# Kernel optimization log

Measured on AMD Instinct MI355X. Metric: run time of the kernel, lower is better.

Reference implementation:

```python
import jax, jax.numpy as jnp
import numpy as np

N = 50000
E = 800000
IN_DIM = 128
HIDDEN = 256
HEADS = 8
HEAD_DIM = HIDDEN // HEADS  # 32
NUM_CLASSES = 40
NEG_SLOPE = 0.2


def setup_inputs() -> dict:
    key = jax.random.key(0)
    ks = jax.random.split(key, 16)
    x = jax.random.normal(ks[0], (N, IN_DIM), dtype=jnp.float32)
    edge_index = jax.random.randint(ks[1], (2, E), 0, N, dtype=jnp.int64)

    def glorot(k, shape, fan_in):
        return jax.random.normal(k, shape, dtype=jnp.float32) / np.sqrt(fan_in)

    # layer 1: in -> heads*head_dim (concat)
    W1 = glorot(ks[2], (IN_DIM, HEADS * HEAD_DIM), IN_DIM)
    as1 = glorot(ks[3], (HEADS, HEAD_DIM), HEAD_DIM)
    ad1 = glorot(ks[4], (HEADS, HEAD_DIM), HEAD_DIM)
    b1 = jnp.zeros((HEADS * HEAD_DIM,), dtype=jnp.float32)
    # layer 2: hidden -> heads*head_dim (concat)
    W2 = glorot(ks[5], (HIDDEN, HEADS * HEAD_DIM), HIDDEN)
    as2 = glorot(ks[6], (HEADS, HEAD_DIM), HEAD_DIM)
    ad2 = glorot(ks[7], (HEADS, HEAD_DIM), HEAD_DIM)
    b2 = jnp.zeros((HEADS * HEAD_DIM,), dtype=jnp.float32)
    # layer 3: hidden -> num_classes, 1 head, no concat (mean == identity for 1 head)
    W3 = glorot(ks[8], (HIDDEN, 1 * NUM_CLASSES), HIDDEN)
    as3 = glorot(ks[9], (1, NUM_CLASSES), NUM_CLASSES)
    ad3 = glorot(ks[10], (1, NUM_CLASSES), NUM_CLASSES)
    b3 = jnp.zeros((NUM_CLASSES,), dtype=jnp.float32)
    return {"x": x, "edge_index": edge_index,
            "W1": W1, "as1": as1, "ad1": ad1, "b1": b1,
            "W2": W2, "as2": as2, "ad2": ad2, "b2": b2,
            "W3": W3, "as3": as3, "ad3": ad3, "b3": b3}


def _segment_softmax(logits, seg, n):
    # logits: [E, H]; softmax per destination node
    m = jax.ops.segment_max(logits, seg, num_segments=n)
    m = jnp.where(jnp.isfinite(m), m, 0.0)  # empty segments -> 0
    e = jnp.exp(logits - m[seg])
    s = jax.ops.segment_sum(e, seg, num_segments=n)
    return e / (s[seg] + 1e-16)


def _gat_layer(x, src, dst, W, a_src, a_dst, b, heads, concat):
    n = x.shape[0]
    h = (x @ W).reshape(n, heads, -1)                    # [N, H, D]
    al_s = jnp.einsum('nhd,hd->nh', h, a_src)            # [N, H]
    al_d = jnp.einsum('nhd,hd->nh', h, a_dst)            # [N, H]
    e = jax.nn.leaky_relu(al_s[src] + al_d[dst], NEG_SLOPE)  # [E, H]
    alpha = _segment_softmax(e, dst, n)                  # [E, H]
    msg = h[src] * alpha[..., None]                      # [E, H, D]
    out = jax.ops.segment_sum(msg, dst, num_segments=n)  # [N, H, D]
    out = out.reshape(n, -1) if concat else out.mean(axis=1)
    return out + b


def reference(x, edge_index, W1, as1, ad1, b1, W2, as2, ad2, b2, W3, as3, ad3, b3):
    # add self loops (PyG GATConv default)
    loops = jnp.arange(N, dtype=edge_index.dtype)
    src = jnp.concatenate([edge_index[0], loops])
    dst = jnp.concatenate([edge_index[1], loops])
    # eval mode: dropout is a no-op
    h = _gat_layer(x, src, dst, W1, as1, ad1, b1, HEADS, True)
    h = jax.nn.elu(h)
    h = _gat_layer(h, src, dst, W2, as2, ad2, b2, HEADS, True)
    h = jax.nn.elu(h)
    out = _gat_layer(h, src, dst, W3, as3, ad3, b3, 1, False)
    return out
```

## Files before the change

kernel.cpp:

```cpp
#include <hip/hip_runtime.h>
#include <hip/hip_bf16.h>

#define NEG_SLOPE 0.2f

typedef __attribute__((ext_vector_type(8))) short bf16x8;
typedef __attribute__((ext_vector_type(4))) float f32x4;

__device__ __forceinline__ unsigned short f2bf(float v) {
    union { float f; unsigned int u; } x; x.f = v;
    unsigned int r = x.u + 0x7fffu + ((x.u >> 16) & 1u);
    return (unsigned short)(r >> 16);
}
__device__ __forceinline__ float bf2f(unsigned short b) {
    union { unsigned int u; float f; } x; x.u = ((unsigned int)b) << 16;
    return x.f;
}


__global__ void count_edges_k(const int* __restrict__ ei, int E, int n, int* __restrict__ cnt) {
    int e = blockIdx.x * 256 + threadIdx.x;
    int ET = E + n;
    if (e >= ET) return;
    int d = (e < E) ? ei[E + e] : (e - E);
    atomicAdd(&cnt[d], 1);
}

__global__ void scan1_k(const int* __restrict__ cnt, int* __restrict__ row_ptr,
                        int* __restrict__ bsums, int n) {
    __shared__ int sd[256];
    int b = blockIdx.x, t = threadIdx.x;
    int base = b * 1024 + t * 4;
    int v[4];
    int loc = 0;
#pragma unroll
    for (int j = 0; j < 4; ++j) {
        v[j] = (base + j < n) ? cnt[base + j] : 0;
        loc += v[j];
    }
    sd[t] = loc;
    __syncthreads();
    for (int off = 1; off < 256; off <<= 1) {
        int x = (t >= off) ? sd[t - off] : 0;
        __syncthreads();
        sd[t] += x;
        __syncthreads();
    }
    int run = sd[t] - loc;
    if (t == 255) bsums[b] = sd[t];
#pragma unroll
    for (int j = 0; j < 4; ++j) {
        if (base + j < n) row_ptr[base + j] = run;
        run += v[j];
    }
}

__global__ void scan2_k(int* __restrict__ bsums, int nb) {
    __shared__ int sd[256];
    int t = threadIdx.x;
    int val = (t < nb) ? bsums[t] : 0;
    sd[t] = val;
    __syncthreads();
    for (int off = 1; off < 256; off <<= 1) {
        int x = (t >= off) ? sd[t - off] : 0;
        __syncthreads();
        sd[t] += x;
        __syncthreads();
    }
    if (t < nb) bsums[t] = sd[t] - val;
}

__global__ void scan3_k(int* __restrict__ row_ptr, int* __restrict__ pos,
                        const int* __restrict__ bsums, int n, int total) {
    int idx = blockIdx.x * 256 + threadIdx.x;
    if (idx < n) {
        int vv = row_ptr[idx] + bsums[idx >> 10];
        row_ptr[idx] = vv;
        pos[idx] = vv;
    } else if (idx == n) {
        row_ptr[n] = total;
    }
}

__global__ void scatter_edges_k(const int* __restrict__ ei, int E, int n,
                                int* __restrict__ pos, int* __restrict__ srcs) {
    int e = blockIdx.x * 256 + threadIdx.x;
    int ET = E + n;
    if (e >= ET) return;
    int s, d;
    if (e < E) { s = ei[e]; d = ei[E + e]; }
    else       { s = e - E; d = e - E; }
    int idx = atomicAdd(&pos[d], 1);
    srcs[idx] = s;
}


#define R1 (128 * 256)
#define R2 (256 * 256)
#define R3 (256 * 128)

__global__ void convert_w_all_k(const float* __restrict__ W1, const float* __restrict__ W2,
                                const float* __restrict__ W3,
                                unsigned short* __restrict__ b1h, unsigned short* __restrict__ b1l,
                                unsigned short* __restrict__ b2h, unsigned short* __restrict__ b2l,
                                unsigned short* __restrict__ b3h, unsigned short* __restrict__ b3l) {
    int idx = blockIdx.x * 256 + threadIdx.x;
    float v;
    unsigned short* dh;
    unsigned short* dl;
    int o;
    if (idx < R1) {
        int k = idx >> 8, c = idx & 255;
        v = W1[idx]; dh = b1h; dl = b1l; o = c * 128 + k;
    } else if (idx < R1 + R2) {
        int j = idx - R1;
        int k = j >> 8, c = j & 255;
        v = W2[j]; dh = b2h; dl = b2l; o = c * 256 + k;
    } else if (idx < R1 + R2 + R3) {
        int j = idx - (R1 + R2);
        int k = j >> 7, c = j & 127;
        v = (c < 40) ? W3[k * 40 + c] : 0.f;
        dh = b3h; dl = b3l; o = c * 256 + k;
    } else {
        return;
    }
    unsigned short h = f2bf(v);
    dh[o] = h;
    dl[o] = f2bf(v - bf2f(h));
}


#define GPAD 40

__global__ __launch_bounds__(256) void mfma_gemm_k(const float* __restrict__ A,
                                                   const unsigned short* __restrict__ Bh,
                                                   const unsigned short* __restrict__ Bl,
                                                   unsigned short* __restrict__ Cb,
                                                   int M, int K, int Nc) {
    __shared__ unsigned short Ash[128][GPAD];
    __shared__ unsigned short Asl[128][GPAD];
    __shared__ unsigned short Bsh[128][GPAD];
    __shared__ unsigned short Bsl[128][GPAD];

    int bm = blockIdx.y * 128;
    int bn = blockIdx.x * 128;
    int t = threadIdx.x;
    int w = t >> 6, l = t & 63;
    int wm = w >> 1, wn = w & 1;
    int lr = l & 15, lk = (l >> 4) * 8;

    int srow = t >> 1;
    int skh  = (t & 1) * 16;

    f32x4 acc[4][4];
#pragma unroll
    for (int i = 0; i < 4; ++i)
#pragma unroll
        for (int j = 0; j < 4; ++j)
            acc[i][j] = (f32x4){0.f, 0.f, 0.f, 0.f};

    const int arow = bm + srow;
    const bool arow_ok = (arow < M);
    const size_t acol_base = (size_t)arow * K + skh;
    const size_t bcol_base = (size_t)(bn + srow) * K + skh;

    for (int k0 = 0; k0 < K; k0 += 32) {
        float vv[16];
        if (arow_ok) {
            const float4* ap = reinterpret_cast<const float4*>(A + acol_base + k0);
#pragma unroll
            for (int q = 0; q < 4; ++q) {
                float4 v4 = ap[q];
                vv[4 * q + 0] = v4.x; vv[4 * q + 1] = v4.y;
                vv[4 * q + 2] = v4.z; vv[4 * q + 3] = v4.w;
            }
        } else {
#pragma unroll
            for (int q = 0; q < 16; ++q) vv[q] = 0.f;
        }
        unsigned int hw[8], lw[8];
#pragma unroll
        for (int q = 0; q < 8; ++q) {
            unsigned short h0 = f2bf(vv[2 * q]);
            unsigned short h1 = f2bf(vv[2 * q + 1]);
            unsigned short l0 = f2bf(vv[2 * q] - bf2f(h0));
            unsigned short l1 = f2bf(vv[2 * q + 1] - bf2f(h1));
            hw[q] = (unsigned int)h0 | ((unsigned int)h1 << 16);
            lw[q] = (unsigned int)l0 | ((unsigned int)l1 << 16);
        }
        __syncthreads();
        {
            uint4* dh = reinterpret_cast<uint4*>(&Ash[srow][skh]);
            uint4* dl = reinterpret_cast<uint4*>(&Asl[srow][skh]);
            dh[0] = make_uint4(hw[0], hw[1], hw[2], hw[3]);
            dh[1] = make_uint4(hw[4], hw[5], hw[6], hw[7]);
            dl[0] = make_uint4(lw[0], lw[1], lw[2], lw[3]);
            dl[1] = make_uint4(lw[4], lw[5], lw[6], lw[7]);
        }
        {
            const uint4* sh = reinterpret_cast<const uint4*>(Bh + bcol_base + k0);
            const uint4* sl = reinterpret_cast<const uint4*>(Bl + bcol_base + k0);
            uint4* dh = reinterpret_cast<uint4*>(&Bsh[srow][skh]);
            uint4* dl = reinterpret_cast<uint4*>(&Bsl[srow][skh]);
            dh[0] = sh[0]; dh[1] = sh[1];
            dl[0] = sl[0]; dl[1] = sl[1];
        }
        __syncthreads();

        bf16x8 ah[4], al[4], bh[4], bl[4];
#pragma unroll
        for (int i = 0; i < 4; ++i) {
            int r = wm * 64 + i * 16 + lr;
            ah[i] = *reinterpret_cast<const bf16x8*>(&Ash[r][lk]);
            al[i] = *reinterpret_cast<const bf16x8*>(&Asl[r][lk]);
        }
#pragma unroll
        for (int j = 0; j < 4; ++j) {
            int c = wn * 64 + j * 16 + lr;
            bh[j] = *reinterpret_cast<const bf16x8*>(&Bsh[c][lk]);
            bl[j] = *reinterpret_cast<const bf16x8*>(&Bsl[c][lk]);
        }
#pragma unroll
        for (int i = 0; i < 4; ++i)
#pragma unroll
            for (int j = 0; j < 4; ++j) {
                acc[i][j] = __builtin_amdgcn_mfma_f32_16x16x32_bf16(ah[i], bh[j], acc[i][j], 0, 0, 0);
                acc[i][j] = __builtin_amdgcn_mfma_f32_16x16x32_bf16(ah[i], bl[j], acc[i][j], 0, 0, 0);
                acc[i][j] = __builtin_amdgcn_mfma_f32_16x16x32_bf16(al[i], bh[j], acc[i][j], 0, 0, 0);
            }
    }

#pragma unroll
    for (int i = 0; i < 4; ++i) {
#pragma unroll
        for (int r = 0; r < 4; ++r) {
            int row_g = bm + wm * 64 + i * 16 + (l >> 4) * 4 + r;
            if (row_g >= M) continue;
#pragma unroll
            for (int j = 0; j < 4; ++j) {
                int col_g = bn + wn * 64 + j * 16 + lr;
                Cb[(size_t)row_g * Nc + col_g] = f2bf(acc[i][j][r]);
            }
        }
    }
}


__global__ __launch_bounds__(256) void gemm_bf16a_k(const unsigned short* __restrict__ A,
                                                    const unsigned short* __restrict__ Bh,
                                                    const unsigned short* __restrict__ Bl,
                                                    unsigned short* __restrict__ Cb,
                                                    int M, int K, int Nc) {
    __shared__ unsigned short As[128][GPAD];
    __shared__ unsigned short Bsh[128][GPAD];
    __shared__ unsigned short Bsl[128][GPAD];

    int bm = blockIdx.y * 128;
    int bn = blockIdx.x * 128;
    int t = threadIdx.x;
    int w = t >> 6, l = t & 63;
    int wm = w >> 1, wn = w & 1;
    int lr = l & 15, lk = (l >> 4) * 8;

    int srow = t >> 1;
    int skh  = (t & 1) * 16;

    f32x4 acc[4][4];
#pragma unroll
    for (int i = 0; i < 4; ++i)
#pragma unroll
        for (int j = 0; j < 4; ++j)
            acc[i][j] = (f32x4){0.f, 0.f, 0.f, 0.f};

    const int arow = bm + srow;
    const bool arow_ok = (arow < M);
    const size_t acol_base = (size_t)arow * K + skh;
    const size_t bcol_base = (size_t)(bn + srow) * K + skh;

    for (int k0 = 0; k0 < K; k0 += 32) {
        __syncthreads();
        {
            uint4* da = reinterpret_cast<uint4*>(&As[srow][skh]);
            if (arow_ok) {
                const uint4* sa = reinterpret_cast<const uint4*>(A + acol_base + k0);
                da[0] = sa[0]; da[1] = sa[1];
            } else {
                da[0] = make_uint4(0u, 0u, 0u, 0u);
                da[1] = make_uint4(0u, 0u, 0u, 0u);
            }
            const uint4* sh = reinterpret_cast<const uint4*>(Bh + bcol_base + k0);
            const uint4* sl = reinterpret_cast<const uint4*>(Bl + bcol_base + k0);
            uint4* dh = reinterpret_cast<uint4*>(&Bsh[srow][skh]);
            uint4* dl = reinterpret_cast<uint4*>(&Bsl[srow][skh]);
            dh[0] = sh[0]; dh[1] = sh[1];
            dl[0] = sl[0]; dl[1] = sl[1];
        }
        __syncthreads();

        bf16x8 ah[4], bh[4], bl[4];
#pragma unroll
        for (int i = 0; i < 4; ++i) {
            int r = wm * 64 + i * 16 + lr;
            ah[i] = *reinterpret_cast<const bf16x8*>(&As[r][lk]);
        }
#pragma unroll
        for (int j = 0; j < 4; ++j) {
            int c = wn * 64 + j * 16 + lr;
            bh[j] = *reinterpret_cast<const bf16x8*>(&Bsh[c][lk]);
            bl[j] = *reinterpret_cast<const bf16x8*>(&Bsl[c][lk]);
        }
#pragma unroll
        for (int i = 0; i < 4; ++i)
#pragma unroll
            for (int j = 0; j < 4; ++j) {
                acc[i][j] = __builtin_amdgcn_mfma_f32_16x16x32_bf16(ah[i], bh[j], acc[i][j], 0, 0, 0);
                acc[i][j] = __builtin_amdgcn_mfma_f32_16x16x32_bf16(ah[i], bl[j], acc[i][j], 0, 0, 0);
            }
    }

#pragma unroll
    for (int i = 0; i < 4; ++i) {
#pragma unroll
        for (int r = 0; r < 4; ++r) {
            int row_g = bm + wm * 64 + i * 16 + (l >> 4) * 4 + r;
            if (row_g >= M) continue;
#pragma unroll
            for (int j = 0; j < 4; ++j) {
                int col_g = bn + wn * 64 + j * 16 + lr;
                Cb[(size_t)row_g * Nc + col_g] = f2bf(acc[i][j][r]);
            }
        }
    }
}


__global__ __launch_bounds__(256) void compute_al_k(const unsigned short* __restrict__ h,
                                                    const float* __restrict__ a_src,
                                                    const float* __restrict__ a_dst,
                                                    float* __restrict__ al_s,
                                                    float* __restrict__ al_d, int n) {
    int gw = blockIdx.x * 4 + (threadIdx.x >> 6);
    int nw = gridDim.x * 4;
    int lane = threadIdx.x & 63;
    float4 asv = reinterpret_cast<const float4*>(a_src)[lane];
    float4 adv = reinterpret_cast<const float4*>(a_dst)[lane];
    for (int node = gw; node < n; node += nw) {
        ushort4 v = reinterpret_cast<const ushort4*>(h + (size_t)node * 256)[lane];
        float ps = bf2f(v.x) * asv.x + bf2f(v.y) * asv.y + bf2f(v.z) * asv.z + bf2f(v.w) * asv.w;
        float pd = bf2f(v.x) * adv.x + bf2f(v.y) * adv.y + bf2f(v.z) * adv.z + bf2f(v.w) * adv.w;
#pragma unroll
        for (int off = 1; off < 8; off <<= 1) {
            ps += __shfl_xor(ps, off, 64);
            pd += __shfl_xor(pd, off, 64);
        }
        if ((lane & 7) == 0) {
            al_s[node * 8 + (lane >> 3)] = ps;
            al_d[node * 8 + (lane >> 3)] = pd;
        }
    }
}

__global__ __launch_bounds__(256) void compute_al3_k(const unsigned short* __restrict__ h,
                                                     const float* __restrict__ a_src,
                                                     const float* __restrict__ a_dst,
                                                     float* __restrict__ al_s,
                                                     float* __restrict__ al_d, int n) {
    int gw = blockIdx.x * 4 + (threadIdx.x >> 6);
    int nw = gridDim.x * 4;
    int lane = threadIdx.x & 63;
    float as = (lane < 40) ? a_src[lane] : 0.f;
    float ad = (lane < 40) ? a_dst[lane] : 0.f;
    for (int node = gw; node < n; node += nw) {
        float hv = (lane < 40) ? bf2f(h[(size_t)node * 128 + lane]) : 0.f;
        float ps = hv * as;
        float pd = hv * ad;
#pragma unroll
        for (int off = 32; off; off >>= 1) {
            ps += __shfl_xor(ps, off, 64);
            pd += __shfl_xor(pd, off, 64);
        }
        if (lane == 0) { al_s[node] = ps; al_d[node] = pd; }
    }
}


__global__ __launch_bounds__(256) void edge_softmax_k(const float* __restrict__ al_s,
                                                      const float* __restrict__ al_d,
                                                      const int* __restrict__ row_ptr,
                                                      const int* __restrict__ srcs,
                                                      float* __restrict__ w,
                                                      float* __restrict__ inv, int n8) {
    int tid = blockIdx.x * 256 + threadIdx.x;
    if (tid >= n8) return;
    int dst = tid >> 3, hd = tid & 7;
    int beg = row_ptr[dst], end = row_ptr[dst + 1];
    float ald = al_d[tid];

    float m = -1e30f;
    int i = beg;
    for (; i + 2 <= end; i += 2) {
        int s0 = srcs[i], s1 = srcs[i + 1];
        float l0 = al_s[s0 * 8 + hd] + ald;
        float l1 = al_s[s1 * 8 + hd] + ald;
        l0 = (l0 > 0.f) ? l0 : NEG_SLOPE * l0;
        l1 = (l1 > 0.f) ? l1 : NEG_SLOPE * l1;
        m = fmaxf(m, fmaxf(l0, l1));
    }
    if (i < end) {
        int s0 = srcs[i];
        float l0 = al_s[s0 * 8 + hd] + ald;
        l0 = (l0 > 0.f) ? l0 : NEG_SLOPE * l0;
        m = fmaxf(m, l0);
    }

    float sw = 0.f;
    i = beg;
    for (; i + 2 <= end; i += 2) {
        int s0 = srcs[i], s1 = srcs[i + 1];
        float l0 = al_s[s0 * 8 + hd] + ald;
        float l1 = al_s[s1 * 8 + hd] + ald;
        l0 = (l0 > 0.f) ? l0 : NEG_SLOPE * l0;
        l1 = (l1 > 0.f) ? l1 : NEG_SLOPE * l1;
        float e0 = __expf(l0 - m);
        float e1 = __expf(l1 - m);
        w[(size_t)i * 8 + hd] = e0;
        w[(size_t)(i + 1) * 8 + hd] = e1;
        sw += e0 + e1;
    }
    if (i < end) {
        int s = srcs[i];
        float l = al_s[s * 8 + hd] + ald;
        l = (l > 0.f) ? l : NEG_SLOPE * l;
        float e = __expf(l - m);
        w[(size_t)i * 8 + hd] = e;
        sw += e;
    }
    inv[tid] = 1.f / (sw + 1e-16f);
}

__global__ __launch_bounds__(256) void edge_softmax3_k(const float* __restrict__ al_s,
                                                       const float* __restrict__ al_d,
                                                       const int* __restrict__ row_ptr,
                                                       const int* __restrict__ srcs,
                                                       float* __restrict__ w,
                                                       float* __restrict__ inv, int n) {
    int dst = blockIdx.x * 256 + threadIdx.x;
    if (dst >= n) return;
    int beg = row_ptr[dst], end = row_ptr[dst + 1];
    float ald = al_d[dst];

    float m = -1e30f;
    int i = beg;
    for (; i + 2 <= end; i += 2) {
        int s0 = srcs[i], s1 = srcs[i + 1];
        float l0 = al_s[s0] + ald;
        float l1 = al_s[s1] + ald;
        l0 = (l0 > 0.f) ? l0 : NEG_SLOPE * l0;
        l1 = (l1 > 0.f) ? l1 : NEG_SLOPE * l1;
        m = fmaxf(m, fmaxf(l0, l1));
    }
    if (i < end) {
        int s0 = srcs[i];
        float l0 = al_s[s0] + ald;
        l0 = (l0 > 0.f) ? l0 : NEG_SLOPE * l0;
        m = fmaxf(m, l0);
    }

    float sw = 0.f;
    for (i = beg; i < end; ++i) {
        int s = srcs[i];
        float l = al_s[s] + ald;
        l = (l > 0.f) ? l : NEG_SLOPE * l;
        float e = __expf(l - m);
        w[i] = e;
        sw += e;
    }
    inv[dst] = 1.f / (sw + 1e-16f);
}


template <bool ELU>
__global__ __launch_bounds__(256) void gat_gather_k(const unsigned short* __restrict__ h,
                                                    const float* __restrict__ w,
                                                    const float* __restrict__ inv,
                                                    const int* __restrict__ row_ptr,
                                                    const int* __restrict__ srcs,
                                                    const float* __restrict__ bias,
                                                    unsigned short* __restrict__ out, int n) {
    int gw = blockIdx.x * 4 + (threadIdx.x >> 6);
    int nw = gridDim.x * 4;
    int lane = threadIdx.x & 63;
    int hd = lane >> 3;
    const ushort4* hp = reinterpret_cast<const ushort4*>(h);
    float4 b4 = reinterpret_cast<const float4*>(bias)[lane];

    for (int dst = gw; dst < n; dst += nw) {
        int beg = row_ptr[dst], end = row_ptr[dst + 1];
        float4 acc = make_float4(0.f, 0.f, 0.f, 0.f);
        int i = beg;
        for (; i + 4 <= end; i += 4) {
            int s0 = srcs[i + 0], s1 = srcs[i + 1], s2 = srcs[i + 2], s3 = srcs[i + 3];
            float w0 = w[(size_t)(i + 0) * 8 + hd];
            float w1 = w[(size_t)(i + 1) * 8 + hd];
            float w2 = w[(size_t)(i + 2) * 8 + hd];
            float w3 = w[(size_t)(i + 3) * 8 + hd];
            ushort4 v0 = hp[(size_t)s0 * 64 + lane];
            ushort4 v1 = hp[(size_t)s1 * 64 + lane];
            ushort4 v2 = hp[(size_t)s2 * 64 + lane];
            ushort4 v3 = hp[(size_t)s3 * 64 + lane];
            acc.x = fmaf(w0, bf2f(v0.x), acc.x);
            acc.y = fmaf(w0, bf2f(v0.y), acc.y);
            acc.z = fmaf(w0, bf2f(v0.z), acc.z);
            acc.w = fmaf(w0, bf2f(v0.w), acc.w);
            acc.x = fmaf(w1, bf2f(v1.x), acc.x);
            acc.y = fmaf(w1, bf2f(v1.y), acc.y);
            acc.z = fmaf(w1, bf2f(v1.z), acc.z);
            acc.w = fmaf(w1, bf2f(v1.w), acc.w);
            acc.x = fmaf(w2, bf2f(v2.x), acc.x);
            acc.y = fmaf(w2, bf2f(v2.y), acc.y);
            acc.z = fmaf(w2, bf2f(v2.z), acc.z);
            acc.w = fmaf(w2, bf2f(v2.w), acc.w);
            acc.x = fmaf(w3, bf2f(v3.x), acc.x);
            acc.y = fmaf(w3, bf2f(v3.y), acc.y);
            acc.z = fmaf(w3, bf2f(v3.z), acc.z);
            acc.w = fmaf(w3, bf2f(v3.w), acc.w);
        }
        for (; i < end; ++i) {
            int s = srcs[i];
            float wgt = w[(size_t)i * 8 + hd];
            ushort4 v = hp[(size_t)s * 64 + lane];
            acc.x = fmaf(wgt, bf2f(v.x), acc.x);
            acc.y = fmaf(wgt, bf2f(v.y), acc.y);
            acc.z = fmaf(wgt, bf2f(v.z), acc.z);
            acc.w = fmaf(wgt, bf2f(v.w), acc.w);
        }

        float iv = inv[dst * 8 + hd];
        float4 o;
        o.x = acc.x * iv + b4.x;
        o.y = acc.y * iv + b4.y;
        o.z = acc.z * iv + b4.z;
        o.w = acc.w * iv + b4.w;
        if (ELU) {
            o.x = (o.x > 0.f) ? o.x : expm1f(o.x);
            o.y = (o.y > 0.f) ? o.y : expm1f(o.y);
            o.z = (o.z > 0.f) ? o.z : expm1f(o.z);
            o.w = (o.w > 0.f) ? o.w : expm1f(o.w);
        }
        ushort4 ob;
        ob.x = f2bf(o.x); ob.y = f2bf(o.y); ob.z = f2bf(o.z); ob.w = f2bf(o.w);
        reinterpret_cast<ushort4*>(out + (size_t)dst * 256)[lane] = ob;
    }
}

__global__ __launch_bounds__(256) void gat_gather3_k(const unsigned short* __restrict__ h,
                                                     const float* __restrict__ w,
                                                     const float* __restrict__ inv,
                                                     const int* __restrict__ row_ptr,
                                                     const int* __restrict__ srcs,
                                                     const float* __restrict__ bias,
                                                     float* __restrict__ out, int n) {
    int gw = blockIdx.x * 4 + (threadIdx.x >> 6);
    int nw = gridDim.x * 4;
    int lane = threadIdx.x & 63;
    int es = lane >> 4, cl = lane & 15;

    for (int dst = gw; dst < n; dst += nw) {
        int beg = row_ptr[dst], end = row_ptr[dst + 1];
        float4 acc = make_float4(0.f, 0.f, 0.f, 0.f);
        for (int i = beg; i < end; i += 4) {
            int idx = i + es;
            bool ok = (idx < end);
            int s = ok ? srcs[idx] : srcs[beg];
            float wgt = ok ? w[idx] : 0.f;
            ushort4 v = reinterpret_cast<const ushort4*>(h + (size_t)s * 128)[cl];
            acc.x = fmaf(wgt, bf2f(v.x), acc.x);
            acc.y = fmaf(wgt, bf2f(v.y), acc.y);
            acc.z = fmaf(wgt, bf2f(v.z), acc.z);
            acc.w = fmaf(wgt, bf2f(v.w), acc.w);
        }
#pragma unroll
        for (int off = 16; off <= 32; off <<= 1) {
            acc.x += __shfl_xor(acc.x, off, 64);
            acc.y += __shfl_xor(acc.y, off, 64);
            acc.z += __shfl_xor(acc.z, off, 64);
            acc.w += __shfl_xor(acc.w, off, 64);
        }
        if (es == 0 && cl < 10) {
            float iv = inv[dst];
            int c = cl * 4;
            float4 b4 = *reinterpret_cast<const float4*>(bias + c);
            float4 o;
            o.x = acc.x * iv + b4.x;
            o.y = acc.y * iv + b4.y;
            o.z = acc.z * iv + b4.z;
            o.w = acc.w * iv + b4.w;
            *reinterpret_cast<float4*>(out + (size_t)dst * 40 + c) = o;
        }
    }
}


extern "C" void kernel_launch(void* const* d_in, const int* in_sizes, int n_in,
                              void* d_out, int out_size, void* d_ws, size_t ws_size,
                              hipStream_t stream) {
    const float* x   = (const float*)d_in[0];
    const int*   ei  = (const int*)d_in[1];
    const float* W1  = (const float*)d_in[2];
    const float* as1 = (const float*)d_in[3];
    const float* ad1 = (const float*)d_in[4];
    const float* b1  = (const float*)d_in[5];
    const float* W2  = (const float*)d_in[6];
    const float* as2 = (const float*)d_in[7];
    const float* ad2 = (const float*)d_in[8];
    const float* b2  = (const float*)d_in[9];
    const float* W3  = (const float*)d_in[10];
    const float* as3 = (const float*)d_in[11];
    const float* ad3 = (const float*)d_in[12];
    const float* b3  = (const float*)d_in[13];

    const int N = in_sizes[0] / 128;
    const int E = in_sizes[1] / 2;
    const int ET = E + N;

    char* ws = (char*)d_ws;
    size_t off = 0;
    auto alloc = [&](size_t bytes) -> void* {
        void* p = ws + off;
        off += (bytes + 255) & ~(size_t)255;
        return p;
    };
    int*   row_ptr = (int*)alloc(sizeof(int) * (N + 1));
    int*   pos     = (int*)alloc(sizeof(int) * N);
    int*   srcs    = (int*)alloc(sizeof(int) * ET);
    int*   bsums   = (int*)alloc(sizeof(int) * 256);
    float* als     = (float*)alloc(sizeof(float) * N * 8);
    float* ald     = (float*)alloc(sizeof(float) * N * 8);
    float* wbuf    = (float*)alloc(sizeof(float) * (size_t)ET * 8);
    float* invb    = (float*)alloc(sizeof(float) * N * 8);
    unsigned short* hb16 = (unsigned short*)alloc(sizeof(unsigned short) * (size_t)N * 256);
    unsigned short* ab16 = (unsigned short*)alloc(sizeof(unsigned short) * (size_t)N * 256);
    unsigned short* wb1h = (unsigned short*)alloc(sizeof(unsigned short) * 128 * 256);
    unsigned short* wb1l = (unsigned short*)alloc(sizeof(unsigned short) * 128 * 256);
    unsigned short* wb2h = (unsigned short*)alloc(sizeof(unsigned short) * 256 * 256);
    unsigned short* wb2l = (unsigned short*)alloc(sizeof(unsigned short) * 256 * 256);
    unsigned short* wb3h = (unsigned short*)alloc(sizeof(unsigned short) * 128 * 256);
    unsigned short* wb3l = (unsigned short*)alloc(sizeof(unsigned short) * 128 * 256);
    (void)ws_size;

    const int nb = (N + 1023) / 1024;
    const int PG = 2048;

    convert_w_all_k<<<(R1 + R2 + R3 + 255) / 256, 256, 0, stream>>>(
        W1, W2, W3, wb1h, wb1l, wb2h, wb2l, wb3h, wb3l);

    hipMemsetAsync(pos, 0, sizeof(int) * N, stream);
    count_edges_k<<<(ET + 255) / 256, 256, 0, stream>>>(ei, E, N, pos);
    scan1_k<<<nb, 256, 0, stream>>>(pos, row_ptr, bsums, N);
    scan2_k<<<1, 256, 0, stream>>>(bsums, nb);
    scan3_k<<<(N + 1 + 255) / 256, 256, 0, stream>>>(row_ptr, pos, bsums, N, ET);
    scatter_edges_k<<<(ET + 255) / 256, 256, 0, stream>>>(ei, E, N, pos, srcs);

    const int gy = (N + 127) / 128;
    const int gsm = (N * 8 + 255) / 256;

    mfma_gemm_k<<<dim3(2, gy), 256, 0, stream>>>(x, wb1h, wb1l, hb16, N, 128, 256);
    compute_al_k<<<PG, 256, 0, stream>>>(hb16, as1, ad1, als, ald, N);
    edge_softmax_k<<<gsm, 256, 0, stream>>>(als, ald, row_ptr, srcs, wbuf, invb, N * 8);
    gat_gather_k<true><<<PG, 256, 0, stream>>>(hb16, wbuf, invb, row_ptr, srcs, b1, ab16, N);

    gemm_bf16a_k<<<dim3(2, gy), 256, 0, stream>>>(ab16, wb2h, wb2l, hb16, N, 256, 256);
    compute_al_k<<<PG, 256, 0, stream>>>(hb16, as2, ad2, als, ald, N);
    edge_softmax_k<<<gsm, 256, 0, stream>>>(als, ald, row_ptr, srcs, wbuf, invb, N * 8);
    gat_gather_k<true><<<PG, 256, 0, stream>>>(hb16, wbuf, invb, row_ptr, srcs, b2, ab16, N);

    gemm_bf16a_k<<<dim3(1, gy), 256, 0, stream>>>(ab16, wb3h, wb3l, hb16, N, 256, 128);
    compute_al3_k<<<PG, 256, 0, stream>>>(hb16, as3, ad3, als, ald, N);
    edge_softmax3_k<<<(N + 255) / 256, 256, 0, stream>>>(als, ald, row_ptr, srcs, wbuf, invb, N);
    gat_gather3_k<<<PG, 256, 0, stream>>>(hb16, wbuf, invb, row_ptr, srcs, b3, (float*)d_out, N);
}
```

Before: 425.4 us.

## Fuse edge softmax into neighbor gather kernels for all GAT layers

Removes the separate edge_softmax kernels and computes attention logits, the segment max, exponentials and normalization inside the gather kernels. Within each wavefront, 8 lanes per head compute edge weights in parallel and broadcast source indices and weights by shuffle, and the 8 neighbor row loads are batched per step. This drops the E×8 weight buffer write and read plus the inverse-sum buffer and three launches, at the cost of reading al_s twice per edge and extra shuffles.

```diff
diff --git a/kernel.cpp b/kernel.cpp
--- a/kernel.cpp
+++ b/kernel.cpp
@@ -383,158 +383,91 @@
 }
 
 
-__global__ __launch_bounds__(256) void edge_softmax_k(const float* __restrict__ al_s,
-                                                      const float* __restrict__ al_d,
-                                                      const int* __restrict__ row_ptr,
-                                                      const int* __restrict__ srcs,
-                                                      float* __restrict__ w,
-                                                      float* __restrict__ inv, int n8) {
-    int tid = blockIdx.x * 256 + threadIdx.x;
-    if (tid >= n8) return;
-    int dst = tid >> 3, hd = tid & 7;
-    int beg = row_ptr[dst], end = row_ptr[dst + 1];
-    float ald = al_d[tid];
-
-    float m = -1e30f;
-    int i = beg;
-    for (; i + 2 <= end; i += 2) {
-        int s0 = srcs[i], s1 = srcs[i + 1];
-        float l0 = al_s[s0 * 8 + hd] + ald;
-        float l1 = al_s[s1 * 8 + hd] + ald;
-        l0 = (l0 > 0.f) ? l0 : NEG_SLOPE * l0;
-        l1 = (l1 > 0.f) ? l1 : NEG_SLOPE * l1;
-        m = fmaxf(m, fmaxf(l0, l1));
-    }
-    if (i < end) {
-        int s0 = srcs[i];
-        float l0 = al_s[s0 * 8 + hd] + ald;
-        l0 = (l0 > 0.f) ? l0 : NEG_SLOPE * l0;
-        m = fmaxf(m, l0);
-    }
-
-    float sw = 0.f;
-    i = beg;
-    for (; i + 2 <= end; i += 2) {
-        int s0 = srcs[i], s1 = srcs[i + 1];
-        float l0 = al_s[s0 * 8 + hd] + ald;
-        float l1 = al_s[s1 * 8 + hd] + ald;
-        l0 = (l0 > 0.f) ? l0 : NEG_SLOPE * l0;
-        l1 = (l1 > 0.f) ? l1 : NEG_SLOPE * l1;
-        float e0 = __expf(l0 - m);
-        float e1 = __expf(l1 - m);
-        w[(size_t)i * 8 + hd] = e0;
-        w[(size_t)(i + 1) * 8 + hd] = e1;
-        sw += e0 + e1;
-    }
-    if (i < end) {
-        int s = srcs[i];
-        float l = al_s[s * 8 + hd] + ald;
-        l = (l > 0.f) ? l : NEG_SLOPE * l;
-        float e = __expf(l - m);
-        w[(size_t)i * 8 + hd] = e;
-        sw += e;
-    }
-    inv[tid] = 1.f / (sw + 1e-16f);
-}
-
-__global__ __launch_bounds__(256) void edge_softmax3_k(const float* __restrict__ al_s,
-                                                       const float* __restrict__ al_d,
-                                                       const int* __restrict__ row_ptr,
-                                                       const int* __restrict__ srcs,
-                                                       float* __restrict__ w,
-                                                       float* __restrict__ inv, int n) {
-    int dst = blockIdx.x * 256 + threadIdx.x;
-    if (dst >= n) return;
-    int beg = row_ptr[dst], end = row_ptr[dst + 1];
-    float ald = al_d[dst];
-
-    float m = -1e30f;
-    int i = beg;
-    for (; i + 2 <= end; i += 2) {
-        int s0 = srcs[i], s1 = srcs[i + 1];
-        float l0 = al_s[s0] + ald;
-        float l1 = al_s[s1] + ald;
-        l0 = (l0 > 0.f) ? l0 : NEG_SLOPE * l0;
-        l1 = (l1 > 0.f) ? l1 : NEG_SLOPE * l1;
-        m = fmaxf(m, fmaxf(l0, l1));
-    }
-    if (i < end) {
-        int s0 = srcs[i];
-        float l0 = al_s[s0] + ald;
-        l0 = (l0 > 0.f) ? l0 : NEG_SLOPE * l0;
-        m = fmaxf(m, l0);
-    }
-
-    float sw = 0.f;
-    for (i = beg; i < end; ++i) {
-        int s = srcs[i];
-        float l = al_s[s] + ald;
-        l = (l > 0.f) ? l : NEG_SLOPE * l;
-        float e = __expf(l - m);
-        w[i] = e;
-        sw += e;
-    }
-    inv[dst] = 1.f / (sw + 1e-16f);
-}
-
-
 template <bool ELU>
-__global__ __launch_bounds__(256) void gat_gather_k(const unsigned short* __restrict__ h,
-                                                    const float* __restrict__ w,
-                                                    const float* __restrict__ inv,
-                                                    const int* __restrict__ row_ptr,
-                                                    const int* __restrict__ srcs,
-                                                    const float* __restrict__ bias,
-                                                    unsigned short* __restrict__ out, int n) {
+__global__ __launch_bounds__(256) void gat_gather_fused_k(const unsigned short* __restrict__ h,
+                                                          const float* __restrict__ al_s,
+                                                          const float* __restrict__ al_d,
+                                                          const int* __restrict__ row_ptr,
+                                                          const int* __restrict__ srcs,
+                                                          const float* __restrict__ bias,
+                                                          unsigned short* __restrict__ out, int n) {
     int gw = blockIdx.x * 4 + (threadIdx.x >> 6);
     int nw = gridDim.x * 4;
     int lane = threadIdx.x & 63;
-    int hd = lane >> 3;
+    int hd = lane >> 3, sl = lane & 7;
+    int gbase = lane & 56;
     const ushort4* hp = reinterpret_cast<const ushort4*>(h);
     float4 b4 = reinterpret_cast<const float4*>(bias)[lane];
 
     for (int dst = gw; dst < n; dst += nw) {
         int beg = row_ptr[dst], end = row_ptr[dst + 1];
+        float ald = al_d[dst * 8 + hd];
+
+        float m = -1e30f;
+        for (int i = beg + sl; i < end; i += 8) {
+            int s = srcs[i];
+            float l = al_s[s * 8 + hd] + ald;
+            l = (l > 0.f) ? l : NEG_SLOPE * l;
+            m = fmaxf(m, l);
+        }
+        m = fmaxf(m, __shfl_xor(m, 1, 64));
+        m = fmaxf(m, __shfl_xor(m, 2, 64));
+        m = fmaxf(m, __shfl_xor(m, 4, 64));
+
         float4 acc = make_float4(0.f, 0.f, 0.f, 0.f);
-        int i = beg;
-        for (; i + 4 <= end; i += 4) {
-            int s0 = srcs[i + 0], s1 = srcs[i + 1], s2 = srcs[i + 2], s3 = srcs[i + 3];
-            float w0 = w[(size_t)(i + 0) * 8 + hd];
-            float w1 = w[(size_t)(i + 1) * 8 + hd];
-            float w2 = w[(size_t)(i + 2) * 8 + hd];
-            float w3 = w[(size_t)(i + 3) * 8 + hd];
-            ushort4 v0 = hp[(size_t)s0 * 64 + lane];
-            ushort4 v1 = hp[(size_t)s1 * 64 + lane];
-            ushort4 v2 = hp[(size_t)s2 * 64 + lane];
-            ushort4 v3 = hp[(size_t)s3 * 64 + lane];
-            acc.x = fmaf(w0, bf2f(v0.x), acc.x);
-            acc.y = fmaf(w0, bf2f(v0.y), acc.y);
-            acc.z = fmaf(w0, bf2f(v0.z), acc.z);
-            acc.w = fmaf(w0, bf2f(v0.w), acc.w);
-            acc.x = fmaf(w1, bf2f(v1.x), acc.x);
-            acc.y = fmaf(w1, bf2f(v1.y), acc.y);
-            acc.z = fmaf(w1, bf2f(v1.z), acc.z);
-            acc.w = fmaf(w1, bf2f(v1.w), acc.w);
-            acc.x = fmaf(w2, bf2f(v2.x), acc.x);
-            acc.y = fmaf(w2, bf2f(v2.y), acc.y);
-            acc.z = fmaf(w2, bf2f(v2.z), acc.z);
-            acc.w = fmaf(w2, bf2f(v2.w), acc.w);
-            acc.x = fmaf(w3, bf2f(v3.x), acc.x);
-            acc.y = fmaf(w3, bf2f(v3.y), acc.y);
-            acc.z = fmaf(w3, bf2f(v3.z), acc.z);
-            acc.w = fmaf(w3, bf2f(v3.w), acc.w);
-        }
-        for (; i < end; ++i) {
-            int s = srcs[i];
-            float wgt = w[(size_t)i * 8 + hd];
-            ushort4 v = hp[(size_t)s * 64 + lane];
-            acc.x = fmaf(wgt, bf2f(v.x), acc.x);
-            acc.y = fmaf(wgt, bf2f(v.y), acc.y);
-            acc.z = fmaf(wgt, bf2f(v.z), acc.z);
-            acc.w = fmaf(wgt, bf2f(v.w), acc.w);
-        }
-
-        float iv = inv[dst * 8 + hd];
+        float sw = 0.f;
+        int nfull = (end - beg) >> 3;
+        int i0 = beg;
+        for (int b = 0; b < nfull; ++b, i0 += 8) {
+            int sE = srcs[i0 + sl];
+            float l = al_s[sE * 8 + hd] + ald;
+            l = (l > 0.f) ? l : NEG_SLOPE * l;
+            float we = __expf(l - m);
+            sw += we;
+            int sj[8];
+            float wj[8];
+#pragma unroll
+            for (int j = 0; j < 8; ++j) {
+                sj[j] = __shfl(sE, gbase + j, 64);
+                wj[j] = __shfl(we, gbase + j, 64);
+            }
+            ushort4 v[8];
+#pragma unroll
+            for (int j = 0; j < 8; ++j) v[j] = hp[(size_t)sj[j] * 64 + lane];
+#pragma unroll
+            for (int j = 0; j < 8; ++j) {
+                acc.x = fmaf(wj[j], bf2f(v[j].x), acc.x);
+                acc.y = fmaf(wj[j], bf2f(v[j].y), acc.y);
+                acc.z = fmaf(wj[j], bf2f(v[j].z), acc.z);
+                acc.w = fmaf(wj[j], bf2f(v[j].w), acc.w);
+            }
+        }
+        int rem = end - i0;
+        if (rem > 0) {
+            int idx = i0 + sl;
+            int sE = srcs[(idx < end) ? idx : (end - 1)];
+            float we = 0.f;
+            if (idx < end) {
+                float l = al_s[sE * 8 + hd] + ald;
+                l = (l > 0.f) ? l : NEG_SLOPE * l;
+                we = __expf(l - m);
+                sw += we;
+            }
+            for (int j = 0; j < rem; ++j) {
+                int sj = __shfl(sE, gbase + j, 64);
+                float wjv = __shfl(we, gbase + j, 64);
+                ushort4 v = hp[(size_t)sj * 64 + lane];
+                acc.x = fmaf(wjv, bf2f(v.x), acc.x);
+                acc.y = fmaf(wjv, bf2f(v.y), acc.y);
+                acc.z = fmaf(wjv, bf2f(v.z), acc.z);
+                acc.w = fmaf(wjv, bf2f(v.w), acc.w);
+            }
+        }
+
+        sw += __shfl_xor(sw, 1, 64);
+        sw += __shfl_xor(sw, 2, 64);
+        sw += __shfl_xor(sw, 4, 64);
+        float iv = 1.f / (sw + 1e-16f);
         float4 o;
         o.x = acc.x * iv + b4.x;
         o.y = acc.y * iv + b4.y;
@@ -552,13 +485,13 @@
     }
 }
 
-__global__ __launch_bounds__(256) void gat_gather3_k(const unsigned short* __restrict__ h,
-                                                     const float* __restrict__ w,
-                                                     const float* __restrict__ inv,
-                                                     const int* __restrict__ row_ptr,
-                                                     const int* __restrict__ srcs,
-                                                     const float* __restrict__ bias,
-                                                     float* __restrict__ out, int n) {
+__global__ __launch_bounds__(256) void gat_gather3_fused_k(const unsigned short* __restrict__ h,
+                                                           const float* __restrict__ al_s,
+                                                           const float* __restrict__ al_d,
+                                                           const int* __restrict__ row_ptr,
+                                                           const int* __restrict__ srcs,
+                                                           const float* __restrict__ bias,
+                                                           float* __restrict__ out, int n) {
     int gw = blockIdx.x * 4 + (threadIdx.x >> 6);
     int nw = gridDim.x * 4;
     int lane = threadIdx.x & 63;
@@ -566,17 +499,36 @@
 
     for (int dst = gw; dst < n; dst += nw) {
         int beg = row_ptr[dst], end = row_ptr[dst + 1];
+        float ald = al_d[dst];
+
+        float m = -1e30f;
+        for (int i = beg + lane; i < end; i += 64) {
+            int s = srcs[i];
+            float l = al_s[s] + ald;
+            l = (l > 0.f) ? l : NEG_SLOPE * l;
+            m = fmaxf(m, l);
+        }
+#pragma unroll
+        for (int off = 32; off; off >>= 1) m = fmaxf(m, __shfl_xor(m, off, 64));
+
         float4 acc = make_float4(0.f, 0.f, 0.f, 0.f);
+        float sw = 0.f;
         for (int i = beg; i < end; i += 4) {
             int idx = i + es;
             bool ok = (idx < end);
             int s = ok ? srcs[idx] : srcs[beg];
-            float wgt = ok ? w[idx] : 0.f;
+            float we = 0.f;
+            if (ok) {
+                float l = al_s[s] + ald;
+                l = (l > 0.f) ? l : NEG_SLOPE * l;
+                we = __expf(l - m);
+                if (cl == 0) sw += we;
+            }
             ushort4 v = reinterpret_cast<const ushort4*>(h + (size_t)s * 128)[cl];
-            acc.x = fmaf(wgt, bf2f(v.x), acc.x);
-            acc.y = fmaf(wgt, bf2f(v.y), acc.y);
-            acc.z = fmaf(wgt, bf2f(v.z), acc.z);
-            acc.w = fmaf(wgt, bf2f(v.w), acc.w);
+            acc.x = fmaf(we, bf2f(v.x), acc.x);
+            acc.y = fmaf(we, bf2f(v.y), acc.y);
+            acc.z = fmaf(we, bf2f(v.z), acc.z);
+            acc.w = fmaf(we, bf2f(v.w), acc.w);
         }
 #pragma unroll
         for (int off = 16; off <= 32; off <<= 1) {
@@ -585,8 +537,11 @@
             acc.z += __shfl_xor(acc.z, off, 64);
             acc.w += __shfl_xor(acc.w, off, 64);
         }
+#pragma unroll
+        for (int off = 1; off <= 32; off <<= 1) sw += __shfl_xor(sw, off, 64);
+
         if (es == 0 && cl < 10) {
-            float iv = inv[dst];
+            float iv = 1.f / (sw + 1e-16f);
             int c = cl * 4;
             float4 b4 = *reinterpret_cast<const float4*>(bias + c);
             float4 o;
@@ -635,8 +590,6 @@
     int*   bsums   = (int*)alloc(sizeof(int) * 256);
     float* als     = (float*)alloc(sizeof(float) * N * 8);
     float* ald     = (float*)alloc(sizeof(float) * N * 8);
-    float* wbuf    = (float*)alloc(sizeof(float) * (size_t)ET * 8);
-    float* invb    = (float*)alloc(sizeof(float) * N * 8);
     unsigned short* hb16 = (unsigned short*)alloc(sizeof(unsigned short) * (size_t)N * 256);
     unsigned short* ab16 = (unsigned short*)alloc(sizeof(unsigned short) * (size_t)N * 256);
     unsigned short* wb1h = (unsigned short*)alloc(sizeof(unsigned short) * 128 * 256);
@@ -661,20 +614,16 @@
     scatter_edges_k<<<(ET + 255) / 256, 256, 0, stream>>>(ei, E, N, pos, srcs);
 
     const int gy = (N + 127) / 128;
-    const int gsm = (N * 8 + 255) / 256;
 
     mfma_gemm_k<<<dim3(2, gy), 256, 0, stream>>>(x, wb1h, wb1l, hb16, N, 128, 256);
     compute_al_k<<<PG, 256, 0, stream>>>(hb16, as1, ad1, als, ald, N);
-    edge_softmax_k<<<gsm, 256, 0, stream>>>(als, ald, row_ptr, srcs, wbuf, invb, N * 8);
-    gat_gather_k<true><<<PG, 256, 0, stream>>>(hb16, wbuf, invb, row_ptr, srcs, b1, ab16, N);
+    gat_gather_fused_k<true><<<PG, 256, 0, stream>>>(hb16, als, ald, row_ptr, srcs, b1, ab16, N);
 
     gemm_bf16a_k<<<dim3(2, gy), 256, 0, stream>>>(ab16, wb2h, wb2l, hb16, N, 256, 256);
     compute_al_k<<<PG, 256, 0, stream>>>(hb16, as2, ad2, als, ald, N);
-    edge_softmax_k<<<gsm, 256, 0, stream>>>(als, ald, row_ptr, srcs, wbuf, invb, N * 8);
-    gat_gather_k<true><<<PG, 256, 0, stream>>>(hb16, wbuf, invb, row_ptr, srcs, b2, ab16, N);
+    gat_gather_fused_k<true><<<PG, 256, 0, stream>>>(hb16, als, ald, row_ptr, srcs, b2, ab16, N);
 
     gemm_bf16a_k<<<dim3(1, gy), 256, 0, stream>>>(ab16, wb3h, wb3l, hb16, N, 256, 128);
     compute_al3_k<<<PG, 256, 0, stream>>>(hb16, as3, ad3, als, ald, N);
-    edge_softmax3_k<<<(N + 255) / 256, 256, 0, stream>>>(als, ald, row_ptr, srcs, wbuf, invb, N);
-    gat_gather3_k<<<PG, 256, 0, stream>>>(hb16, wbuf, invb, row_ptr, srcs, b3, (float*)d_out, N);
-}
+    gat_gather3_fused_k<<<PG, 256, 0, stream>>>(hb16, als, ald, row_ptr, srcs, b3, (float*)d_out, N);
+}
```

After: 413.4 us. -2.8%, faster.
